# Performance work log

Hardware: AMD Instinct MI355X
Metric: run time of the kernel (lower is better)

The kernel has to match this reference:

```python
import jax, jax.numpy as jnp
import numpy as np

B, S, H, L = 256, 128, 1024, 2
FEATS = {"t": 300, "v": 35, "a": 74}


def setup_inputs() -> dict:
    key = jax.random.key(0)
    inp = {}
    k = 0

    def nk():
        nonlocal k
        k += 1
        return jax.random.fold_in(key, k)

    inp["t_input"] = jax.random.normal(nk(), (B, S, FEATS["t"]), jnp.float32)
    inp["v_input"] = jax.random.normal(nk(), (B, S, FEATS["v"]), jnp.float32)
    inp["a_input"] = jax.random.normal(nk(), (B, S, FEATS["a"]), jnp.float32)
    std = 1.0 / np.sqrt(H)
    for m, f in FEATS.items():
        in_sizes = [f + 2 * H, H]  # layer0 gets modality feat + two cross-modal hiddens
        for l in range(L):
            inp[f"Wih_{m}{l}"] = jax.random.normal(nk(), (4 * H, in_sizes[l]), jnp.float32) * std
            inp[f"Whh_{m}{l}"] = jax.random.normal(nk(), (4 * H, H), jnp.float32) * std
            inp[f"bih_{m}{l}"] = jax.random.normal(nk(), (4 * H,), jnp.float32) * std
            inp[f"bhh_{m}{l}"] = jax.random.normal(nk(), (4 * H,), jnp.float32) * std
    inp["Wd"] = jax.random.normal(nk(), (1, 3 * H), jnp.float32) * np.sqrt(2.0 / (1 + 3 * H))
    inp["bd"] = jnp.zeros((1,), jnp.float32)
    return inp


def _cell(x, h, c, Wih, Whh, bih, bhh):
    # PyTorch LSTM gate order: i, f, g, o
    z = x @ Wih.T + h @ Whh.T + bih + bhh  # [B, 4H]
    i, f, g, o = jnp.split(z, 4, axis=-1)
    c_new = jax.nn.sigmoid(f) * c + jax.nn.sigmoid(i) * jnp.tanh(g)
    h_new = jax.nn.sigmoid(o) * jnp.tanh(c_new)
    return h_new, c_new


def _stack_cell(x, hs, cs, layers):
    new_h, new_c = [], []
    inp = x
    for l, (Wih, Whh, bih, bhh) in enumerate(layers):
        h, c = _cell(inp, hs[l], cs[l], Wih, Whh, bih, bhh)
        new_h.append(h)
        new_c.append(c)
        inp = h
    return jnp.stack(new_h), jnp.stack(new_c)


def _forward(t_input, v_input, a_input, pt, pv, pa, Wd, bd):
    z = jnp.zeros((L, B, H), t_input.dtype)
    carry0 = (z, z, z, z, z, z)
    xs = (t_input.transpose(1, 0, 2), v_input.transpose(1, 0, 2), a_input.transpose(1, 0, 2))

    def step(carry, x):
        ht, ct, hv, cv, ha, ca = carry
        xt, xv, xa = x
        tf, vf, af = ht[-1], hv[-1], ha[-1]  # top-layer hiddens from previous step
        t_in = jnp.concatenate([xt, vf, af], axis=-1)
        v_in = jnp.concatenate([xv, tf, af], axis=-1)
        a_in = jnp.concatenate([xa, tf, vf], axis=-1)
        ht, ct = _stack_cell(t_in, ht, ct, pt)
        hv, cv = _stack_cell(v_in, hv, cv, pv)
        ha, ca = _stack_cell(a_in, ha, ca, pa)
        return (ht, ct, hv, cv, ha, ca), None

    (ht, ct, hv, cv, ha, ca), _ = jax.lax.scan(step, carry0, xs)
    feat = jnp.concatenate([ht[-1], hv[-1], ha[-1]], axis=-1)  # [B, 3H]
    return feat @ Wd.T + bd  # [B, 1]


def reference(t_input, v_input, a_input,
              Wih_t0, Whh_t0, bih_t0, bhh_t0, Wih_t1, Whh_t1, bih_t1, bhh_t1,
              Wih_v0, Whh_v0, bih_v0, bhh_v0, Wih_v1, Whh_v1, bih_v1, bhh_v1,
              Wih_a0, Whh_a0, bih_a0, bhh_a0, Wih_a1, Whh_a1, bih_a1, bhh_a1,
              Wd, bd):
    pt = [(Wih_t0, Whh_t0, bih_t0, bhh_t0), (Wih_t1, Whh_t1, bih_t1, bhh_t1)]
    pv = [(Wih_v0, Whh_v0, bih_v0, bhh_v0), (Wih_v1, Whh_v1, bih_v1, bhh_v1)]
    pa = [(Wih_a0, Whh_a0, bih_a0, bhh_a0), (Wih_a1, Whh_a1, bih_a1, bhh_a1)]
    return _forward(t_input, v_input, a_input, pt, pv, pa, Wd, bd)
```

## Files before the change

kernel.cpp:

```cpp
#include <hip/hip_runtime.h>
#include <hip/hip_fp16.h>
#include <cstdint>
#include <cstddef>


typedef _Float16 half8 __attribute__((ext_vector_type(8)));
typedef float floatx4 __attribute__((ext_vector_type(4)));

__device__ __forceinline__ void gload16(const void* g, void* l) {
  __builtin_amdgcn_global_load_lds(
      (const __attribute__((address_space(1))) void*)g,
      (__attribute__((address_space(3))) void*)l, 16, 0, 0);
}

__device__ __forceinline__ float fsig(float x) {
  return 1.f / (1.f + __expf(-x));
}
__device__ __forceinline__ float ftanhf(float x) {
  x = fminf(15.f, fmaxf(-15.f, x));
  float e = __expf(2.f * x);
  return (e - 1.f) / (e + 1.f);
}

struct ModParam {
  const __half* xseg;
  const __half* inseg;
  const __half* W;
  const float* bias;
  float* c;
  __half* dst0; __half* dst1; __half* dst2;
  int off0, off1, off2;
  __half* feat; int featoff;
  int Kx, Kin;
};
struct PhaseParams { ModParam m[3]; };

__global__ __launch_bounds__(256, 3) void lstm_phase(PhaseParams P) {
  const int b_ = blockIdx.x;
  const int xcd = b_ & 7, rnd = b_ >> 3;
  const int pairIdx = xcd * 24 + (rnd >> 2);
  const int mt = rnd & 3;
  const int mod = pairIdx >> 6;
  const int bn = pairIdx & 63;
  const ModParam p = P.m[mod];
  const int nKt = (p.Kx + p.Kin) >> 7;
  const int KxT = p.Kx >> 7;
  const int tid = threadIdx.x;
  const int lane = tid & 63, wid = tid >> 6;
  const int ln = lane & 15, lm = lane >> 4, c4 = lane & 3;

  __shared__ __align__(16) __half smem[2][1024][8];

  floatx4 acc[4][4];
#pragma unroll
  for (int a = 0; a < 4; ++a)
#pragma unroll
    for (int b = 0; b < 4; ++b) acc[a][b] = (floatx4)0.f;

  half8 bvA[4], bvB[4];

  auto stageA = [&](int kt, int buf) {
    const __half* base; int kq0;
    if (kt < KxT) { base = p.xseg;  kq0 = kt * 16; }
    else          { base = p.inseg; kq0 = (kt - KxT) * 16; }
#pragma unroll
    for (int it = 0; it < 4; ++it) {
      int idx = it * 256 + tid;
      int kql = idx >> 6, bl = idx & 63;
      gload16(base + ((size_t)(kq0 + kql) * 256 + mt * 64 + bl) * 8,
              &smem[buf][idx][0]);
    }
  };
  auto loadB = [&](int kt, half8 (&bv)[4]) {
    const __half* src =
        p.W + ((size_t)(bn * nKt + kt) * 4 + wid) * 2048 + lane * 8;
#pragma unroll
    for (int ni = 0; ni < 4; ++ni) bv[ni] = *(const half8*)(src + ni * 512);
  };
  auto compute = [&](int buf, const half8 (&bv)[4]) {
    half8 av[4];
    const int kq = wid * 4 + lm;
#pragma unroll
    for (int mi = 0; mi < 4; ++mi)
      av[mi] = *(const half8*)&smem[buf][kq * 64 + mi * 16 + ln][0];
#pragma unroll
    for (int mi = 0; mi < 4; ++mi)
#pragma unroll
      for (int ni = 0; ni < 4; ++ni)
        acc[mi][ni] = __builtin_amdgcn_mfma_f32_16x16x32_f16(
            av[mi], bv[ni], acc[mi][ni], 0, 0, 0);
  };

  loadB(0, bvA);
  stageA(0, 0);
  __syncthreads();
  int kt = 0;
  while (true) {
    if (kt + 1 < nKt) { loadB(kt + 1, bvB); stageA(kt + 1, 1); }
    compute(0, bvA);
    __syncthreads();
    if (++kt >= nKt) break;
    if (kt + 1 < nKt) { loadB(kt + 1, bvA); stageA(kt + 1, 0); }
    compute(1, bvB);
    __syncthreads();
    if (++kt >= nKt) break;
  }

  floatx4* rbuf = (floatx4*)&smem[0][0][0];
  auto slot = [&](int h, int ni, int w) {
    return ((h * 4 + ni) * 4 + w) * 64 + lane;
  };
  floatx4 own[4];
#pragma unroll
  for (int ni = 0; ni < 4; ++ni) {
    rbuf[slot(0, ni, wid)] = acc[0][ni];
    rbuf[slot(1, ni, wid)] = acc[1][ni];
  }
  __syncthreads();
  if (wid == 0) {
#pragma unroll
    for (int ni = 0; ni < 4; ++ni)
      own[ni] = acc[0][ni] + rbuf[slot(0, ni, 1)] + rbuf[slot(0, ni, 2)] +
                rbuf[slot(0, ni, 3)];
  } else if (wid == 1) {
#pragma unroll
    for (int ni = 0; ni < 4; ++ni)
      own[ni] = acc[1][ni] + rbuf[slot(1, ni, 0)] + rbuf[slot(1, ni, 2)] +
                rbuf[slot(1, ni, 3)];
  }
  __syncthreads();
#pragma unroll
  for (int ni = 0; ni < 4; ++ni) {
    rbuf[slot(0, ni, wid)] = acc[2][ni];
    rbuf[slot(1, ni, wid)] = acc[3][ni];
  }
  __syncthreads();
  if (wid == 2) {
#pragma unroll
    for (int ni = 0; ni < 4; ++ni)
      own[ni] = acc[2][ni] + rbuf[slot(0, ni, 0)] + rbuf[slot(0, ni, 1)] +
                rbuf[slot(0, ni, 3)];
  } else if (wid == 3) {
#pragma unroll
    for (int ni = 0; ni < 4; ++ni)
      own[ni] = acc[3][ni] + rbuf[slot(1, ni, 0)] + rbuf[slot(1, ni, 1)] +
                rbuf[slot(1, ni, 2)];
  }

#pragma unroll
  for (int ni = 0; ni < 4; ++ni) {
    const int ncol = bn * 64 + ni * 16 + ln;
    const float bia = p.bias[ncol];
    const int j = ncol >> 2;
#pragma unroll
    for (int r = 0; r < 4; ++r) {
      float v = own[ni][r] + bia;
      float g1 = __shfl_xor(v, 1);
      float g2 = __shfl_xor(v, 2);
      float g3 = __shfl_xor(v, 3);
      int m0 = c4, m1 = c4 ^ 1, m2 = c4 ^ 2, m3 = c4 ^ 3;
      float zi = m0 == 0 ? v : (m0 == 1 ? g1 : (m0 == 2 ? g2 : g3));
      float zf = m1 == 0 ? v : (m1 == 1 ? g1 : (m1 == 2 ? g2 : g3));
      float zg = m2 == 0 ? v : (m2 == 1 ? g1 : (m2 == 2 ? g2 : g3));
      float zo = m3 == 0 ? v : (m3 == 1 ? g1 : (m3 == 2 ? g2 : g3));
      const int b = mt * 64 + wid * 16 + lm * 4 + r;
      float cp = p.c[b * 1024 + j];
      float cn = fsig(zf) * cp + fsig(zi) * ftanhf(zg);
      float hn = fsig(zo) * ftanhf(cn);
      __half h16 = __float2half(hn);
      if (c4 == 0) {
        if (p.dst0) {
          int col = p.off0 + j;
          p.dst0[(size_t)(col >> 3) * 2048 + b * 8 + (col & 7)] = h16;
        }
      } else if (c4 == 1) {
        if (p.dst1) {
          int col = p.off1 + j;
          p.dst1[(size_t)(col >> 3) * 2048 + b * 8 + (col & 7)] = h16;
        }
      } else if (c4 == 2) {
        if (p.dst2) {
          int col = p.off2 + j;
          p.dst2[(size_t)(col >> 3) * 2048 + b * 8 + (col & 7)] = h16;
        }
      } else {
        p.c[b * 1024 + j] = cn;
        if (p.feat) p.feat[(size_t)b * 3072 + p.featoff + j] = h16;
      }
    }
  }
}

__global__ void pack_w(__half* dst, const float* Wih, const float* Whh,
                       float* bdst, const float* bih, const float* bhh,
                       int f, int fpad, int hih, int Ktot) {
  long long i = (long long)blockIdx.x * 256 + threadIdx.x;
  long long tot = (long long)4096 * Ktot;
  const int nKt = Ktot >> 7;
  if (i < tot) {
    int q = (int)(i >> 11);
    int wid = q & 3;
    int p2 = q >> 2;
    int ktile = p2 % nKt, nt = p2 / nKt;
    int r = (int)(i & 2047);
    int ni = r >> 9, lane = (r >> 3) & 63, e = r & 7;
    int n = nt * 64 + ni * 16 + (lane & 15);
    int nsrc = (n & 3) * 1024 + (n >> 2);
    int k = ktile * 128 + wid * 32 + (lane >> 4) * 8 + e;
    float v;
    if (k < fpad)
      v = (k < f) ? Wih[(size_t)nsrc * (f + hih) + k] : 0.f;
    else if (k < fpad + hih)
      v = Wih[(size_t)nsrc * (f + hih) + f + (k - fpad)];
    else
      v = Whh[(size_t)nsrc * 1024 + (k - fpad - hih)];
    dst[i] = __float2half(v);
  }
  if (i < 4096) {
    int nsrc = ((int)i & 3) * 1024 + ((int)i >> 2);
    bdst[i] = bih[nsrc] + bhh[nsrc];
  }
}

__global__ void pack_x(__half* dst, const float* x, int f, int fpad) {
  long long i = (long long)blockIdx.x * 256 + threadIdx.x;
  long long tot = (long long)128 * 256 * fpad;
  if (i >= tot) return;
  int e = (int)(i & 7);
  long long u = i >> 3;
  int b = (int)(u & 255);
  long long v = u >> 8;
  int nq = fpad >> 3;
  int kq = (int)(v % nq);
  int t = (int)(v / nq);
  int k = kq * 8 + e;
  dst[i] = (k < f) ? __float2half(x[((size_t)b * 128 + t) * f + k])
                   : __float2half(0.f);
}

__global__ void final_dot(const __half* feat, const float* Wd, const float* bd,
                          float* out) {
  int b = blockIdx.x, tid = threadIdx.x;
  float s = 0.f;
  for (int j = tid; j < 3072; j += 256)
    s += __half2float(feat[(size_t)b * 3072 + j]) * Wd[j];
  __shared__ float red[256];
  red[tid] = s;
  __syncthreads();
  for (int o = 128; o > 0; o >>= 1) {
    if (tid < o) red[tid] += red[tid + o];
    __syncthreads();
  }
  if (tid == 0) out[b] = red[0] + bd[0];
}

extern "C" void kernel_launch(void* const* d_in, const int* in_sizes, int n_in,
                              void* d_out, int out_size, void* d_ws, size_t ws_size,
                              hipStream_t stream) {
  const int B = 256, S = 128, H = 1024, NG = 4096;
  const int FRAW[3] = {300, 35, 74};
  const int FPAD[3] = {384, 128, 128};

  const float* xin[3] = {(const float*)d_in[0], (const float*)d_in[1],
                         (const float*)d_in[2]};
  const float *Wih0[3], *Whh0[3], *bih0[3], *bhh0[3];
  const float *Wih1[3], *Whh1[3], *bih1[3], *bhh1[3];
  for (int m = 0; m < 3; ++m) {
    int bidx = 3 + m * 8;
    Wih0[m] = (const float*)d_in[bidx + 0];
    Whh0[m] = (const float*)d_in[bidx + 1];
    bih0[m] = (const float*)d_in[bidx + 2];
    bhh0[m] = (const float*)d_in[bidx + 3];
    Wih1[m] = (const float*)d_in[bidx + 4];
    Whh1[m] = (const float*)d_in[bidx + 5];
    bih1[m] = (const float*)d_in[bidx + 6];
    bhh1[m] = (const float*)d_in[bidx + 7];
  }
  const float* Wd = (const float*)d_in[27];
  const float* bd = (const float*)d_in[28];

  uint8_t* wsb = (uint8_t*)d_ws;
  size_t off = 0;
  auto alloc = [&](size_t bytes) -> void* {
    void* p = wsb + off;
    off += (bytes + 255) & ~(size_t)255;
    return p;
  };

  __half* W0[3];
  __half* W1[3];
  int K0[3];
  for (int m = 0; m < 3; ++m) {
    K0[m] = FPAD[m] + 3 * H;
    W0[m] = (__half*)alloc((size_t)NG * K0[m] * 2);
  }
  for (int m = 0; m < 3; ++m) W1[m] = (__half*)alloc((size_t)NG * 2 * H * 2);
  float* biasB = (float*)alloc((size_t)6 * NG * 4);
  __half* X16[3];
  for (int m = 0; m < 3; ++m)
    X16[m] = (__half*)alloc((size_t)S * B * FPAD[m] * 2);
  size_t stateStart = off;
  __half* In0[3];
  __half* In1[3];
  for (int m = 0; m < 3; ++m) In0[m] = (__half*)alloc((size_t)2 * B * 3072 * 2);
  for (int m = 0; m < 3; ++m) In1[m] = (__half*)alloc((size_t)2 * B * 2048 * 2);
  float* cbuf = (float*)alloc((size_t)6 * B * H * 4);
  size_t stateEnd = off;
  __half* featB = (__half*)alloc((size_t)B * 3072 * 2);

  if (off > ws_size) return;

  for (int m = 0; m < 3; ++m) {
    long long tot0 = (long long)NG * K0[m];
    pack_w<<<dim3((unsigned)((tot0 + 255) / 256)), 256, 0, stream>>>(
        W0[m], Wih0[m], Whh0[m], biasB + m * NG, bih0[m], bhh0[m],
        FRAW[m], FPAD[m], 2 * H, K0[m]);
    long long tot1 = (long long)NG * 2 * H;
    pack_w<<<dim3((unsigned)((tot1 + 255) / 256)), 256, 0, stream>>>(
        W1[m], Wih1[m], Whh1[m], biasB + (3 + m) * NG, bih1[m], bhh1[m],
        0, 0, H, 2 * H);
    long long totx = (long long)S * B * FPAD[m];
    pack_x<<<dim3((unsigned)((totx + 255) / 256)), 256, 0, stream>>>(
        X16[m], xin[m], FRAW[m], FPAD[m]);
  }
  hipMemsetAsync(wsb + stateStart, 0, stateEnd - stateStart, stream);

  for (int t = 0; t < S; ++t) {
    int pq = t & 1;
    __half* in0cur[3], *in0nxt[3], *in1cur[3], *in1nxt[3];
    for (int m = 0; m < 3; ++m) {
      in0cur[m] = In0[m] + (size_t)pq * B * 3072;
      in0nxt[m] = In0[m] + (size_t)(pq ^ 1) * B * 3072;
      in1cur[m] = In1[m] + (size_t)pq * B * 2048;
      in1nxt[m] = In1[m] + (size_t)(pq ^ 1) * B * 2048;
    }

    PhaseParams PA;
    for (int m = 0; m < 3; ++m) {
      ModParam& q = PA.m[m];
      q.xseg = X16[m] + (size_t)t * B * FPAD[m];
      q.Kx = FPAD[m];
      q.inseg = in0cur[m];
      q.Kin = 3072;
      q.W = W0[m];
      q.bias = biasB + m * NG;
      q.c = cbuf + (size_t)m * B * H;
      q.dst0 = in1cur[m]; q.off0 = 0;
      q.dst1 = in0nxt[m]; q.off1 = 2048;
      q.dst2 = nullptr;   q.off2 = 0;
      q.feat = nullptr;   q.featoff = 0;
    }
    lstm_phase<<<dim3(768), 256, 0, stream>>>(PA);

    PhaseParams PB;
    for (int m = 0; m < 3; ++m) {
      ModParam& q = PB.m[m];
      q.xseg = nullptr; q.Kx = 0;
      q.inseg = in1cur[m]; q.Kin = 2048;
      q.W = W1[m];
      q.bias = biasB + (3 + m) * NG;
      q.c = cbuf + (size_t)(3 + m) * B * H;
      q.feat = (t == S - 1) ? featB : nullptr;
      q.featoff = m * H;
      if (m == 0) {
        q.dst0 = in0nxt[1]; q.off0 = 0;
        q.dst1 = in0nxt[2]; q.off1 = 0;
        q.dst2 = in1nxt[0]; q.off2 = 1024;
      } else if (m == 1) {
        q.dst0 = in0nxt[0]; q.off0 = 0;
        q.dst1 = in0nxt[2]; q.off1 = 1024;
        q.dst2 = in1nxt[1]; q.off2 = 1024;
      } else {
        q.dst0 = in0nxt[0]; q.off0 = 1024;
        q.dst1 = in0nxt[1]; q.off1 = 1024;
        q.dst2 = in1nxt[2]; q.off2 = 1024;
      }
    }
    lstm_phase<<<dim3(768), 256, 0, stream>>>(PB);
  }

  final_dot<<<dim3(256), 256, 0, stream>>>(featB, Wd, bd, (float*)d_out);
}
```

Before: 9.950 ms.

## Halve batch tile per block and double grid to raise occupancy

Each LSTM phase block now covers 32 batch rows instead of 64, so the grid doubles to 1536 blocks and launch bounds rise to 6 blocks per CU. Shared memory and accumulator registers are halved, and the cross-wave reduction plus gate epilogue are reorganised so each wave owns one 16-column slice. The aim is more parallelism and latency hiding on the small per-step GEMMs. The cost is that each weight tile is now read by twice as many blocks, doubling weight traffic.

Result: slower. 10.56 ms (+6.1%).

```diff
diff --git a/kernel.cpp b/kernel.cpp
--- a/kernel.cpp
+++ b/kernel.cpp
@@ -12,7 +12,6 @@
       (const __attribute__((address_space(1))) void*)g,
       (__attribute__((address_space(3))) void*)l, 16, 0, 0);
 }
-
 __device__ __forceinline__ float fsig(float x) {
   return 1.f / (1.f + __expf(-x));
 }
@@ -35,11 +34,11 @@
 };
 struct PhaseParams { ModParam m[3]; };
 
-__global__ __launch_bounds__(256, 3) void lstm_phase(PhaseParams P) {
+__global__ __launch_bounds__(256, 6) void lstm_phase(PhaseParams P) {
   const int b_ = blockIdx.x;
   const int xcd = b_ & 7, rnd = b_ >> 3;
-  const int pairIdx = xcd * 24 + (rnd >> 2);
-  const int mt = rnd & 3;
+  const int pairIdx = xcd * 24 + (rnd >> 3);
+  const int mt = rnd & 7;
   const int mod = pairIdx >> 6;
   const int bn = pairIdx & 63;
   const ModParam p = P.m[mod];
@@ -49,11 +48,11 @@
   const int lane = tid & 63, wid = tid >> 6;
   const int ln = lane & 15, lm = lane >> 4, c4 = lane & 3;
 
-  __shared__ __align__(16) __half smem[2][1024][8];
-
-  floatx4 acc[4][4];
-#pragma unroll
-  for (int a = 0; a < 4; ++a)
+  __shared__ __align__(16) __half smem[2][512][8];
+
+  floatx4 acc[2][4];
+#pragma unroll
+  for (int a = 0; a < 2; ++a)
 #pragma unroll
     for (int b = 0; b < 4; ++b) acc[a][b] = (floatx4)0.f;
 
@@ -64,10 +63,10 @@
     if (kt < KxT) { base = p.xseg;  kq0 = kt * 16; }
     else          { base = p.inseg; kq0 = (kt - KxT) * 16; }
 #pragma unroll
-    for (int it = 0; it < 4; ++it) {
+    for (int it = 0; it < 2; ++it) {
       int idx = it * 256 + tid;
-      int kql = idx >> 6, bl = idx & 63;
-      gload16(base + ((size_t)(kq0 + kql) * 256 + mt * 64 + bl) * 8,
+      int kql = idx >> 5, row = idx & 31;
+      gload16(base + ((size_t)(kq0 + kql) * 256 + mt * 32 + row) * 8,
               &smem[buf][idx][0]);
     }
   };
@@ -78,13 +77,13 @@
     for (int ni = 0; ni < 4; ++ni) bv[ni] = *(const half8*)(src + ni * 512);
   };
   auto compute = [&](int buf, const half8 (&bv)[4]) {
-    half8 av[4];
+    half8 av[2];
     const int kq = wid * 4 + lm;
 #pragma unroll
-    for (int mi = 0; mi < 4; ++mi)
-      av[mi] = *(const half8*)&smem[buf][kq * 64 + mi * 16 + ln][0];
-#pragma unroll
-    for (int mi = 0; mi < 4; ++mi)
+    for (int mi = 0; mi < 2; ++mi)
+      av[mi] = *(const half8*)&smem[buf][kq * 32 + mi * 16 + ln][0];
+#pragma unroll
+    for (int mi = 0; mi < 2; ++mi)
 #pragma unroll
       for (int ni = 0; ni < 4; ++ni)
         acc[mi][ni] = __builtin_amdgcn_mfma_f32_16x16x32_f16(
@@ -107,54 +106,26 @@
   }
 
   floatx4* rbuf = (floatx4*)&smem[0][0][0];
-  auto slot = [&](int h, int ni, int w) {
-    return ((h * 4 + ni) * 4 + w) * 64 + lane;
-  };
-  floatx4 own[4];
-#pragma unroll
-  for (int ni = 0; ni < 4; ++ni) {
-    rbuf[slot(0, ni, wid)] = acc[0][ni];
-    rbuf[slot(1, ni, wid)] = acc[1][ni];
-  }
-  __syncthreads();
-  if (wid == 0) {
-#pragma unroll
-    for (int ni = 0; ni < 4; ++ni)
-      own[ni] = acc[0][ni] + rbuf[slot(0, ni, 1)] + rbuf[slot(0, ni, 2)] +
-                rbuf[slot(0, ni, 3)];
-  } else if (wid == 1) {
-#pragma unroll
-    for (int ni = 0; ni < 4; ++ni)
-      own[ni] = acc[1][ni] + rbuf[slot(1, ni, 0)] + rbuf[slot(1, ni, 2)] +
-                rbuf[slot(1, ni, 3)];
-  }
-  __syncthreads();
-#pragma unroll
-  for (int ni = 0; ni < 4; ++ni) {
-    rbuf[slot(0, ni, wid)] = acc[2][ni];
-    rbuf[slot(1, ni, wid)] = acc[3][ni];
-  }
-  __syncthreads();
-  if (wid == 2) {
-#pragma unroll
-    for (int ni = 0; ni < 4; ++ni)
-      own[ni] = acc[2][ni] + rbuf[slot(0, ni, 0)] + rbuf[slot(0, ni, 1)] +
-                rbuf[slot(0, ni, 3)];
-  } else if (wid == 3) {
-#pragma unroll
-    for (int ni = 0; ni < 4; ++ni)
-      own[ni] = acc[3][ni] + rbuf[slot(1, ni, 0)] + rbuf[slot(1, ni, 1)] +
-                rbuf[slot(1, ni, 2)];
-  }
-
-#pragma unroll
-  for (int ni = 0; ni < 4; ++ni) {
-    const int ncol = bn * 64 + ni * 16 + ln;
-    const float bia = p.bias[ncol];
-    const int j = ncol >> 2;
+  auto slot = [&](int ni, int w) { return (ni * 4 + w) * 64 + lane; };
+  floatx4 own[2];
+#pragma unroll
+  for (int mi = 0; mi < 2; ++mi) {
+    __syncthreads();
+#pragma unroll
+    for (int ni = 0; ni < 4; ++ni) rbuf[slot(ni, wid)] = acc[mi][ni];
+    __syncthreads();
+    own[mi] = rbuf[slot(wid, 0)] + rbuf[slot(wid, 1)] + rbuf[slot(wid, 2)] +
+              rbuf[slot(wid, 3)];
+  }
+
+  const int ncol = bn * 64 + wid * 16 + ln;
+  const float bia = p.bias[ncol];
+  const int j = ncol >> 2;
+#pragma unroll
+  for (int mi = 0; mi < 2; ++mi) {
 #pragma unroll
     for (int r = 0; r < 4; ++r) {
-      float v = own[ni][r] + bia;
+      float v = own[mi][r] + bia;
       float g1 = __shfl_xor(v, 1);
       float g2 = __shfl_xor(v, 2);
       float g3 = __shfl_xor(v, 3);
@@ -163,7 +134,7 @@
       float zf = m1 == 0 ? v : (m1 == 1 ? g1 : (m1 == 2 ? g2 : g3));
       float zg = m2 == 0 ? v : (m2 == 1 ? g1 : (m2 == 2 ? g2 : g3));
       float zo = m3 == 0 ? v : (m3 == 1 ? g1 : (m3 == 2 ? g2 : g3));
-      const int b = mt * 64 + wid * 16 + lm * 4 + r;
+      const int b = mt * 32 + mi * 16 + lm * 4 + r;
       float cp = p.c[b * 1024 + j];
       float cn = fsig(zf) * cp + fsig(zi) * ftanhf(zg);
       float hn = fsig(zo) * ftanhf(cn);
@@ -350,7 +321,7 @@
       q.dst2 = nullptr;   q.off2 = 0;
       q.feat = nullptr;   q.featoff = 0;
     }
-    lstm_phase<<<dim3(768), 256, 0, stream>>>(PA);
+    lstm_phase<<<dim3(1536), 256, 0, stream>>>(PA);
 
     PhaseParams PB;
     for (int m = 0; m < 3; ++m) {
@@ -376,7 +347,7 @@
         q.dst2 = in1nxt[2]; q.off2 = 1024;
       }
     }
-    lstm_phase<<<dim3(768), 256, 0, stream>>>(PB);
+    lstm_phase<<<dim3(1536), 256, 0, stream>>>(PB);
   }
 
   final_dot<<<dim3(256), 256, 0, stream>>>(featB, Wd, bd, (float*)d_out);
```
